# Optimization experiments

Hardware: AMD Instinct MI355X
Metric: run time of the kernel (lower is better)

## Reference

```python
import jax, jax.numpy as jnp
import numpy as np

PAD, UNK, START = 0, 1, 2
V, E, H = 32000, 256, 512   # vocab, emb dim, encoder hidden per direction
H2 = 2 * H                   # decoder hidden / encoder output dim
B, L, T = 32, 400, 64
OOV = 100


def _lstm(xe, Wi, Wh, b, reverse=False):
    """xe: [B,L,E] -> (hs [B,L,H], h_last [B,H])."""
    Bb = xe.shape[0]
    Hh = Wh.shape[0]
    def step(carry, xt):
        h, c = carry
        z = xt @ Wi + h @ Wh + b
        i, fg, g, o = jnp.split(z, 4, axis=-1)
        c = jax.nn.sigmoid(fg) * c + jax.nn.sigmoid(i) * jnp.tanh(g)
        h = jax.nn.sigmoid(o) * jnp.tanh(c)
        return (h, c), h
    init = (jnp.zeros((Bb, Hh), xe.dtype), jnp.zeros((Bb, Hh), xe.dtype))
    (hN, _), hs = jax.lax.scan(step, init, jnp.swapaxes(xe, 0, 1), reverse=reverse)
    return jnp.swapaxes(hs, 0, 1), hN


def _gru(x, h, Wi, Wh, b):
    D = h.shape[-1]
    zi = x @ Wi + b
    zh = h @ Wh
    r = jax.nn.sigmoid(zi[:, :D] + zh[:, :D])
    z = jax.nn.sigmoid(zi[:, D:2 * D] + zh[:, D:2 * D])
    n = jnp.tanh(zi[:, 2 * D:] + r * zh[:, 2 * D:])
    return (1.0 - z) * n + z * h


def _forward(embedding, enc_Wi_f, enc_Wh_f, enc_b_f, enc_Wi_b, enc_Wh_b, enc_b_b,
             dec_Wi, dec_Wh, dec_b, W_enc_att, W_dec_att, Wv, bv, Wp, bp,
             x, target_y, extend_vocab):
    Bb, Ll = x.shape
    Tt = target_y.shape[1]
    Vv = embedding.shape[0]
    Hh2 = dec_Wh.shape[0]
    xe = embedding[x]                                           # B,L,E
    hs_f, hN_f = _lstm(xe, enc_Wi_f, enc_Wh_f, enc_b_f)
    hs_b, hN_b = _lstm(xe, enc_Wi_b, enc_Wh_b, enc_b_b, reverse=True)
    enc_out = jnp.concatenate([hs_f, hs_b], axis=-1)            # B,L,2H
    dec_h0 = jnp.concatenate([hN_f, hN_b], axis=-1)             # B,2H
    bidx = jnp.arange(Bb)[:, None]

    def step(carry, inp):
        dec_in, dec_h, acc, prebuf = carry
        i, tgt = inp
        emb = embedding[dec_in]                                 # B,E
        dec_h = _gru(emb, dec_h, dec_Wi, dec_Wh, dec_b)         # B,2H
        # temporal encoder attention (normalize exp scores by running sum)
        e = jnp.einsum('bh,hk,blk->bl', dec_h, W_enc_att, enc_out)
        ee = jnp.exp(e)
        att_un = jnp.where(i == 0, ee, ee / (acc + 1e-10))
        acc = acc + ee
        enc_att = att_un / jnp.sum(att_un, axis=-1, keepdims=True)   # B,L
        enc_ctx = jnp.einsum('bl,blh->bh', enc_att, enc_out)
        # intra-decoder attention over previous decoder hiddens
        ed = jnp.einsum('bh,hk,btk->bt', dec_h, W_dec_att, prebuf)
        dmask = (jnp.arange(prebuf.shape[1]) < i)[None, :]
        dec_att = jax.nn.softmax(jnp.where(dmask, ed, -1e9), axis=-1)
        dec_ctx = jnp.einsum('bt,bth->bh', dec_att, prebuf)
        dec_ctx = jnp.where(i > 0, dec_ctx, 0.0)
        cat = jnp.concatenate([dec_h, enc_ctx, dec_ctx], axis=-1)    # B,6H
        p_gen = jax.nn.sigmoid(cat @ Wp + bp)                        # B,1
        ptr_dist = p_gen * enc_att                                   # B,L
        vocab_dist = (1.0 - p_gen) * jax.nn.softmax(cat @ Wv + bv, axis=-1)
        final = jnp.zeros((Bb, Vv + OOV), vocab_dist.dtype)
        final = final.at[:, :Vv].set(vocab_dist)
        final = final.at[bidx, extend_vocab].add(ptr_dist)           # copy mechanism
        dec_out = jnp.argmax(final, axis=-1)
        step_loss = -jnp.log(final[jnp.arange(Bb), tgt] + 1e-12)
        step_loss = step_loss * (tgt != PAD).astype(final.dtype)
        prebuf = jax.lax.dynamic_update_slice(prebuf, dec_h[:, None, :], (0, i, 0))
        nxt = jnp.where(dec_out >= Vv, UNK, dec_out).astype(dec_in.dtype)
        return (nxt, dec_h, acc, prebuf), (dec_out, step_loss)

    init = (jnp.full((Bb,), START, dtype=x.dtype), dec_h0,
            jnp.zeros((Bb, Ll), enc_out.dtype),
            jnp.zeros((Bb, Tt, Hh2), enc_out.dtype))
    _, (ys, losses) = jax.lax.scan(step, init, (jnp.arange(Tt), target_y.T))
    return jnp.swapaxes(ys, 0, 1), jnp.swapaxes(losses, 0, 1)


def setup_inputs() -> dict:
    key = jax.random.key(0)
    ks = jax.random.split(key, 16)
    s = 0.02
    nrm = lambda k, shape: jax.random.normal(k, shape, jnp.float32) * s
    return {
        'x': jax.random.randint(ks[0], (B, L), 0, V),
        'seq_len': L,
        'target_y': jax.random.randint(ks[1], (B, T), 0, V),
        'extend_vocab': jax.random.randint(ks[2], (B, L), 0, V + OOV),
        'max_ovv_len': OOV,
        'embedding': nrm(ks[3], (V, E)),
        'enc_Wi_f': nrm(ks[4], (E, 4 * H)),
        'enc_Wh_f': nrm(ks[5], (H, 4 * H)),
        'enc_b_f': jnp.zeros((4 * H,), jnp.float32),
        'enc_Wi_b': nrm(ks[6], (E, 4 * H)),
        'enc_Wh_b': nrm(ks[7], (H, 4 * H)),
        'enc_b_b': jnp.zeros((4 * H,), jnp.float32),
        'dec_Wi': nrm(ks[8], (E, 3 * H2)),
        'dec_Wh': nrm(ks[9], (H2, 3 * H2)),
        'dec_b': jnp.zeros((3 * H2,), jnp.float32),
        'W_enc_att': nrm(ks[10], (H2, H2)),
        'W_dec_att': nrm(ks[11], (H2, H2)),
        'Wv': nrm(ks[12], (3 * H2, V)),
        'bv': jnp.zeros((V,), jnp.float32),
        'Wp': nrm(ks[13], (3 * H2, 1)),
        'bp': jnp.zeros((1,), jnp.float32),
    }


def reference(x, seq_len, target_y, extend_vocab, max_ovv_len,
              embedding, enc_Wi_f, enc_Wh_f, enc_b_f, enc_Wi_b, enc_Wh_b, enc_b_b,
              dec_Wi, dec_Wh, dec_b, W_enc_att, W_dec_att, Wv, bv, Wp, bp):
    return _forward(embedding, enc_Wi_f, enc_Wh_f, enc_b_f, enc_Wi_b, enc_Wh_b, enc_b_b,
                    dec_Wi, dec_Wh, dec_b, W_enc_att, W_dec_att, Wv, bv, Wp, bp,
                    x, target_y, extend_vocab)
```

## Files before the change

kernel.cpp:

```cpp
#include <hip/hip_runtime.h>
#include <math.h>

#define Bb 32
#define Lmax 400
#define Tt 64
#define Ee 256
#define Hh 512
#define H2 1024
#define Vv 32000
#define OOV 100
#define VX (Vv+OOV)
#define PAD_ID 0
#define UNK_ID 1
#define START_ID 2

__device__ __forceinline__ float sigf(float x){ return 1.0f/(1.0f+expf(-x)); }
__device__ __forceinline__ float bf2f(unsigned int u){ u <<= 16; return __uint_as_float(u); }

__global__ __launch_bounds__(256) void pack_enc_k(
    const float* __restrict__ Wi_f, const float* __restrict__ Wh_f, const float* __restrict__ b_f,
    const float* __restrict__ Wi_b, const float* __restrict__ Wh_b, const float* __restrict__ b_b,
    float4* __restrict__ wip, float4* __restrict__ whp, float4* __restrict__ bp)
{
  int o = blockIdx.x*256 + threadIdx.x;
  if (o < 2*256*512) {
    int n = o & 511; int k = (o >> 9) & 255; int dir = o >> 17;
    const float* W = dir ? Wi_b : Wi_f;
    wip[o] = make_float4(W[k*2048+n], W[k*2048+512+n], W[k*2048+1024+n], W[k*2048+1536+n]);
  }
  if (o < 2*512*512) {
    int n = o & 511; int k = (o >> 9) & 511; int dir = o >> 18;
    const float* W = dir ? Wh_b : Wh_f;
    whp[o] = make_float4(W[k*2048+n], W[k*2048+512+n], W[k*2048+1024+n], W[k*2048+1536+n]);
  }
  if (o < 2*512) {
    int n = o & 511; int dir = o >> 9;
    const float* bs = dir ? b_b : b_f;
    bp[o] = make_float4(bs[n], bs[512+n], bs[1024+n], bs[1536+n]);
  }
}

#define FMA16(ACC, HV, W0, W1, W2, W3) \
  ACC.x = fmaf(HV.x, W0.x, ACC.x); ACC.y = fmaf(HV.x, W0.y, ACC.y); \
  ACC.z = fmaf(HV.x, W0.z, ACC.z); ACC.w = fmaf(HV.x, W0.w, ACC.w); \
  ACC.x = fmaf(HV.y, W1.x, ACC.x); ACC.y = fmaf(HV.y, W1.y, ACC.y); \
  ACC.z = fmaf(HV.y, W1.z, ACC.z); ACC.w = fmaf(HV.y, W1.w, ACC.w); \
  ACC.x = fmaf(HV.z, W2.x, ACC.x); ACC.y = fmaf(HV.z, W2.y, ACC.y); \
  ACC.z = fmaf(HV.z, W2.z, ACC.z); ACC.w = fmaf(HV.z, W2.w, ACC.w); \
  ACC.x = fmaf(HV.w, W3.x, ACC.x); ACC.y = fmaf(HV.w, W3.y, ACC.y); \
  ACC.z = fmaf(HV.w, W3.z, ACC.z); ACC.w = fmaf(HV.w, W3.w, ACC.w);

__global__ __launch_bounds__(512) void enc_step3_k(
    const float4* __restrict__ wip, const float4* __restrict__ whp, const float4* __restrict__ bp,
    const float* __restrict__ emb, const int* __restrict__ x,
    float* __restrict__ c_buf, float* __restrict__ enc_out, int t)
{
  __shared__ float4 wi_s[256*4];
  __shared__ float4 wh_s[512*4];
  __shared__ float4 hs2[128*33];
  __shared__ float4 xr_red[64*33];
  int bx = blockIdx.x;
  int dir = bx >> 7, ng = bx & 127;
  int tid = threadIdx.x;
  int ks = tid >> 5;
  int r  = tid & 31;
  int bq = r & 7, nl = r >> 3;
  int b0 = bq*4;
  int tt = dir ? (Lmax-1-t) : t;

  for (int i = tid; i < 1024; i += 512) {
    int k = i >> 2, l = i & 3;
    wi_s[i] = wip[(dir*256 + k)*512 + ng*4 + l];
  }
  for (int i = tid; i < 2048; i += 512) {
    int k = i >> 2, l = i & 3;
    wh_s[i] = whp[(dir*512 + k)*512 + ng*4 + l];
  }
  {
    int sb = tid >> 4, kb = tid & 15;
    int tok = x[sb*Lmax + tt];
    const float4* er = (const float4*)(emb + (size_t)tok*Ee);
    #pragma unroll
    for (int i = 0; i < 4; ++i) {
      int k4 = kb + 16*i;
      xr_red[k4*33 + sb] = er[k4];
    }
  }
  if (t > 0) {
    int pt = dir ? (tt+1) : (tt-1);
    int sb = tid >> 4, kb = tid & 15;
    const float4* hb = (const float4*)(enc_out + ((size_t)sb*Lmax + pt)*H2 + dir*Hh);
    #pragma unroll
    for (int i = 0; i < 8; ++i) {
      int k4 = kb + 16*i;
      hs2[k4*33 + sb] = hb[k4];
    }
  }
  __syncthreads();

  float4 acc0 = make_float4(0.f,0.f,0.f,0.f);
  float4 acc1 = acc0, acc2 = acc0, acc3 = acc0;
  if (t > 0) {
    int k4b = ks*8;
    #pragma unroll
    for (int kk = 0; kk < 8; ++kk) {
      int k4 = k4b + kk;
      float4 w0 = wh_s[(k4*4+0)*4 + nl];
      float4 w1 = wh_s[(k4*4+1)*4 + nl];
      float4 w2 = wh_s[(k4*4+2)*4 + nl];
      float4 w3 = wh_s[(k4*4+3)*4 + nl];
      float4 h0 = hs2[k4*33 + b0+0];
      float4 h1 = hs2[k4*33 + b0+1];
      float4 h2 = hs2[k4*33 + b0+2];
      float4 h3 = hs2[k4*33 + b0+3];
      FMA16(acc0, h0, w0, w1, w2, w3);
      FMA16(acc1, h1, w0, w1, w2, w3);
      FMA16(acc2, h2, w0, w1, w2, w3);
      FMA16(acc3, h3, w0, w1, w2, w3);
    }
  }
  {
    int k4b = ks*4;
    #pragma unroll
    for (int kk = 0; kk < 4; ++kk) {
      int k4 = k4b + kk;
      float4 w0 = wi_s[(k4*4+0)*4 + nl];
      float4 w1 = wi_s[(k4*4+1)*4 + nl];
      float4 w2 = wi_s[(k4*4+2)*4 + nl];
      float4 w3 = wi_s[(k4*4+3)*4 + nl];
      float4 h0 = xr_red[k4*33 + b0+0];
      float4 h1 = xr_red[k4*33 + b0+1];
      float4 h2 = xr_red[k4*33 + b0+2];
      float4 h3 = xr_red[k4*33 + b0+3];
      FMA16(acc0, h0, w0, w1, w2, w3);
      FMA16(acc1, h1, w0, w1, w2, w3);
      FMA16(acc2, h2, w0, w1, w2, w3);
      FMA16(acc3, h3, w0, w1, w2, w3);
    }
  }
  __syncthreads();
  {
    int base = ks*132 + 16*bq + nl;
    xr_red[base + 0]  = acc0;
    xr_red[base + 4]  = acc1;
    xr_red[base + 8]  = acc2;
    xr_red[base + 12] = acc3;
  }
  __syncthreads();
  if (tid < 128) {
    int bn = tid;
    float4 s = xr_red[bn];
    #pragma unroll
    for (int kr = 1; kr < 16; ++kr) {
      float4 v = xr_red[kr*132 + bn];
      s.x += v.x; s.y += v.y; s.z += v.z; s.w += v.w;
    }
    int b = bn >> 2, nl2 = bn & 3, n = ng*4 + nl2;
    float4 bb = bp[dir*512 + n];
    float zi = s.x + bb.x;
    float zf = s.y + bb.y;
    float zg = s.z + bb.z;
    float zo = s.w + bb.w;
    int ci = (dir*32 + b)*Hh + n;
    float cv = (t==0) ? 0.f : c_buf[ci];
    float cn = sigf(zf)*cv + sigf(zi)*tanhf(zg);
    float hn = sigf(zo)*tanhf(cn);
    c_buf[ci] = cn;
    enc_out[((size_t)b*Lmax + tt)*H2 + dir*Hh + n] = hn;
  }
}

__global__ __launch_bounds__(256) void init_dec_k(
    const float* __restrict__ enc_out, float* __restrict__ cat_buf,
    float* __restrict__ h0, int* __restrict__ dec_in)
{
  int idx = blockIdx.x*256 + threadIdx.x;
  if (idx < Bb*H2) {
    int b = idx >> 10, n = idx & 1023;
    float v = (n < Hh) ? enc_out[((size_t)b*Lmax + (Lmax-1))*H2 + n]
                       : enc_out[(size_t)b*Lmax*H2 + n];
    cat_buf[b*3*H2 + n] = v;
    h0[b*H2 + n] = v;
  }
  if (idx < Bb) dec_in[idx] = START_ID;
}

__global__ __launch_bounds__(256) void gru_mm_k(
    const float* __restrict__ emb, const int* __restrict__ dec_in,
    const float* __restrict__ cat_buf, const float* __restrict__ Wi,
    const float* __restrict__ Wh, const float* __restrict__ bias,
    float* __restrict__ zi_buf, float* __restrict__ zh_buf)
{
  int bx = blockIdx.x;
  int ng = bx % 48; int bg = (bx / 48) & 7; int kq = bx / 384;
  int nl = threadIdx.x & 63, bl = threadIdx.x >> 6;
  int n = ng*64 + nl, b = bg*4 + bl;
  const float* hr = cat_buf + b*3*H2;
  float zh = 0.f;
  int k0 = kq*512;
  #pragma unroll 4
  for (int k = k0; k < k0+512; ++k)
    zh = fmaf(hr[k], Wh[(size_t)k*3*H2 + n], zh);
  zh_buf[(size_t)(kq*Bb + b)*3*H2 + n] = zh;
  if (kq == 0) {
    const float* er = emb + (size_t)dec_in[b]*Ee;
    float zi = bias[n];
    #pragma unroll 4
    for (int k = 0; k < Ee; ++k)
      zi = fmaf(er[k], Wi[(size_t)k*3*H2 + n], zi);
    zi_buf[b*3*H2 + n] = zi;
  }
}

__global__ __launch_bounds__(256) void qq_f_k(
    const float* __restrict__ zi_buf, const float* __restrict__ zh_buf,
    const float* __restrict__ h0, float* __restrict__ prebuf,
    const float* __restrict__ Wea, const float* __restrict__ Wda,
    float* __restrict__ cat_buf, float* __restrict__ qp, float* __restrict__ qdp, int t)
{
  __shared__ float hsq[4*260];
  int bx = blockIdx.x;
  int ng = bx & 15, bg = (bx >> 4) & 7, kq = bx >> 7;
  int nl = threadIdx.x & 63, bl = threadIdx.x >> 6;
  int n = ng*64 + nl, b = bg*4 + bl;
  const float* zi  = zi_buf + b*3*H2;
  const float* zh0 = zh_buf + (size_t)b*3*H2;
  const float* zh1 = zh_buf + (size_t)(Bb + b)*3*H2;
  #pragma unroll
  for (int i = 0; i < 4; ++i) {
    int kk = nl + 64*i, k = kq*256 + kk;
    float zhr = zh0[k]      + zh1[k];
    float zhz = zh0[H2+k]   + zh1[H2+k];
    float zhg = zh0[2*H2+k] + zh1[2*H2+k];
    float rr = sigf(zi[k] + zhr);
    float zz = sigf(zi[H2+k] + zhz);
    float nn = tanhf(zi[2*H2+k] + rr*zhg);
    float hold = (t == 0) ? h0[b*H2 + k]
                          : prebuf[((size_t)b*Tt + (t-1))*H2 + k];
    float h = (1.0f - zz)*nn + zz*hold;
    hsq[bl*260 + kk] = h;
    if (ng == 0) {
      cat_buf[b*3*H2 + k] = h;
      prebuf[((size_t)b*Tt + t)*H2 + k] = h;
    }
  }
  __syncthreads();
  const float* hr = hsq + bl*260;
  const float* wa = Wea + (size_t)(kq*256)*H2 + n;
  const float* wd = Wda + (size_t)(kq*256)*H2 + n;
  float s1 = 0.f, s2 = 0.f;
  #pragma unroll 4
  for (int kk = 0; kk < 256; ++kk) {
    float hv = hr[kk];
    s1 = fmaf(hv, wa[(size_t)kk*H2], s1);
    s2 = fmaf(hv, wd[(size_t)kk*H2], s2);
  }
  qp [(size_t)(kq*Bb + b)*H2 + n] = s1;
  qdp[(size_t)(kq*Bb + b)*H2 + n] = s2;
}

__global__ __launch_bounds__(256) void qsum_k(
    const float* __restrict__ qp, const float* __restrict__ qdp,
    float* __restrict__ q, float* __restrict__ qd)
{
  int i = blockIdx.x*256 + threadIdx.x;
  const float4* p  = (const float4*)qp;
  const float4* pd = (const float4*)qdp;
  float4 a = p[i], b1 = p[8192+i], c = p[16384+i], d = p[24576+i];
  ((float4*)q)[i] = make_float4(a.x+b1.x+c.x+d.x, a.y+b1.y+c.y+d.y,
                                a.z+b1.z+c.z+d.z, a.w+b1.w+c.w+d.w);
  float4 e = pd[i], f = pd[8192+i], g = pd[16384+i], h = pd[24576+i];
  ((float4*)qd)[i] = make_float4(e.x+f.x+g.x+h.x, e.y+f.y+g.y+h.y,
                                 e.z+f.z+g.z+h.z, e.w+f.w+g.w+h.w);
}

__global__ __launch_bounds__(256) void att_sc_k(
    const float* __restrict__ q, const float* __restrict__ qd,
    const float* __restrict__ enc_out, const float* __restrict__ prebuf,
    float* __restrict__ esc, float* __restrict__ ed, int t)
{
  int w = blockIdx.x*4 + (threadIdx.x >> 6);
  int lane = threadIdx.x & 63;
  int b = w / 464;
  int row = w - b*464;
  if (b >= Bb) return;
  float s = 0.0f;
  if (row < Lmax) {
    const float4* qr = (const float4*)(q + b*H2);
    const float4* er = (const float4*)(enc_out + ((size_t)b*Lmax + row)*H2);
    #pragma unroll
    for (int j = 0; j < 4; ++j) {
      float4 a = qr[lane + 64*j], e = er[lane + 64*j];
      s += a.x*e.x + a.y*e.y + a.z*e.z + a.w*e.w;
    }
  } else {
    int tp = row - Lmax;
    if (tp >= t) { if (lane==0) ed[b*Tt+tp] = 0.0f; return; }
    const float4* qr = (const float4*)(qd + b*H2);
    const float4* pr = (const float4*)(prebuf + ((size_t)b*Tt + tp)*H2);
    #pragma unroll
    for (int j = 0; j < 4; ++j) {
      float4 a = qr[lane + 64*j], e = pr[lane + 64*j];
      s += a.x*e.x + a.y*e.y + a.z*e.z + a.w*e.w;
    }
  }
  for (int o = 32; o > 0; o >>= 1) s += __shfl_xor(s, o);
  if (lane == 0) { if (row < Lmax) esc[b*Lmax+row] = s; else ed[b*Tt + (row-Lmax)] = s; }
}

__global__ __launch_bounds__(256) void ctx_norm_k(
    const float* __restrict__ esc, const float* __restrict__ acc_r, float* __restrict__ acc_w,
    float* __restrict__ enc_att, const float* __restrict__ ed,
    const float* __restrict__ enc_out, const float* __restrict__ prebuf,
    float* __restrict__ cat_buf, int t)
{
  __shared__ float att_s[Lmax];
  __shared__ float datt_s[Tt];
  __shared__ float red[256];
  int b = blockIdx.x >> 4, kq = blockIdx.x & 15;
  int tid = threadIdx.x;
  float loc = 0.f;
  for (int l = tid; l < Lmax; l += 256) {
    float ee = expf(esc[b*Lmax + l]);
    float a  = (t == 0) ? 0.f : acc_r[b*Lmax + l];
    float un = (t == 0) ? ee : ee / (a + 1e-10f);
    att_s[l] = un;
    loc += un;
    if (kq == 0) acc_w[b*Lmax + l] = a + ee;
  }
  red[tid] = loc; __syncthreads();
  for (int s = 128; s > 0; s >>= 1) { if (tid < s) red[tid] += red[tid+s]; __syncthreads(); }
  float inv = 1.0f / red[0];
  for (int l = tid; l < Lmax; l += 256) {
    float v = att_s[l] * inv;
    att_s[l] = v;
    if (kq == 0) enc_att[b*Lmax + l] = v;
  }
  if (tid < 64 && t > 0) {
    float v = (tid < t) ? ed[b*Tt + tid] : -INFINITY;
    float m = v;
    for (int o = 32; o > 0; o >>= 1) m = fmaxf(m, __shfl_xor(m, o));
    float p = (tid < t) ? expf(v - m) : 0.f;
    float ss = p;
    for (int o = 32; o > 0; o >>= 1) ss += __shfl_xor(ss, o);
    datt_s[tid] = p / ss;
  }
  __syncthreads();
  int k = kq*64 + (tid & 63);
  int strip = tid >> 6;
  float ec = 0.f;
  const float* er = enc_out + (size_t)b*Lmax*H2 + k;
  #pragma unroll 4
  for (int l = strip; l < Lmax; l += 4)
    ec = fmaf(att_s[l], er[(size_t)l*H2], ec);
  float dc = 0.f;
  const float* pr = prebuf + (size_t)b*Tt*H2 + k;
  for (int tp = strip; tp < t; tp += 4)
    dc = fmaf(datt_s[tp], pr[(size_t)tp*H2], dc);
  __syncthreads();
  red[tid] = ec; __syncthreads();
  if (tid < 64)
    cat_buf[b*3*H2 + H2 + kq*64 + tid] = red[tid] + red[64+tid] + red[128+tid] + red[192+tid];
  __syncthreads();
  red[tid] = dc; __syncthreads();
  if (tid < 64)
    cat_buf[b*3*H2 + 2*H2 + kq*64 + tid] = red[tid] + red[64+tid] + red[128+tid] + red[192+tid];
}

__global__ __launch_bounds__(256) void pack_wv_k(const float* __restrict__ Wv, unsigned short* __restrict__ Wbf)
{
  size_t i = ((size_t)blockIdx.x*256 + threadIdx.x)*4;
  #pragma unroll
  for (int j = 0; j < 4; ++j) {
    unsigned int u = __float_as_uint(Wv[i+j]);
    u = (u + 0x7fffu + ((u >> 16) & 1u)) >> 16;
    Wbf[i+j] = (unsigned short)u;
  }
}

__global__ __launch_bounds__(256) void wv_mm_bf_k(
    const float* __restrict__ cat_buf, const unsigned short* __restrict__ Wbf,
    const float* __restrict__ bv, float* __restrict__ logits)
{
  __shared__ float As[32][33];
  __shared__ float Wsh[32][65];
  int tid = threadIdx.x;
  int n0 = blockIdx.x*64;
  int tx = tid & 15, ty = tid >> 4;
  float acc[2][4] = {};
  for (int k0 = 0; k0 < 3*H2; k0 += 32) {
    #pragma unroll
    for (int i = 0; i < 4; ++i) {
      int a = tid*4+i;
      As[a>>5][a&31] = cat_buf[(size_t)(a>>5)*3*H2 + k0 + (a&31)];
    }
    #pragma unroll
    for (int j = 0; j < 4; ++j) {
      int a = j*256 + tid;
      int row = a >> 5, c2 = (a & 31)*2;
      const unsigned int* wr = (const unsigned int*)(Wbf + (size_t)(k0+row)*Vv + n0);
      unsigned int u = wr[a & 31];
      Wsh[row][c2]   = bf2f(u & 0xffffu);
      Wsh[row][c2+1] = bf2f(u >> 16);
    }
    __syncthreads();
    #pragma unroll
    for (int kk = 0; kk < 32; ++kk) {
      float a0 = As[ty*2+0][kk], a1 = As[ty*2+1][kk];
      float w0 = Wsh[kk][tx*4+0], w1 = Wsh[kk][tx*4+1], w2 = Wsh[kk][tx*4+2], w3 = Wsh[kk][tx*4+3];
      acc[0][0]=fmaf(a0,w0,acc[0][0]); acc[0][1]=fmaf(a0,w1,acc[0][1]); acc[0][2]=fmaf(a0,w2,acc[0][2]); acc[0][3]=fmaf(a0,w3,acc[0][3]);
      acc[1][0]=fmaf(a1,w0,acc[1][0]); acc[1][1]=fmaf(a1,w1,acc[1][1]); acc[1][2]=fmaf(a1,w2,acc[1][2]); acc[1][3]=fmaf(a1,w3,acc[1][3]);
    }
    __syncthreads();
  }
  #pragma unroll
  for (int i = 0; i < 2; ++i)
    #pragma unroll
    for (int j = 0; j < 4; ++j) {
      int n = n0 + tx*4 + j;
      logits[(size_t)(ty*2+i)*Vv + n] = acc[i][j] + bv[n];
    }
}

__global__ __launch_bounds__(256) void wv_mm_k(
    const float* __restrict__ cat_buf, const float* __restrict__ Wv,
    const float* __restrict__ bv, float* __restrict__ logits)
{
  __shared__ float As[32][33];
  __shared__ float Wsh[32][128];
  int tid = threadIdx.x;
  int n0 = blockIdx.x*128;
  int tx = tid & 31, ty = tid >> 5;
  float acc[4][4] = {};
  for (int k0 = 0; k0 < 3*H2; k0 += 32) {
    #pragma unroll
    for (int i = 0; i < 4; ++i) {
      int a = tid*4+i;
      As[a>>5][a&31] = cat_buf[(size_t)(a>>5)*3*H2 + k0 + (a&31)];
    }
    #pragma unroll
    for (int j = 0; j < 16; ++j) {
      int a = j*256+tid;
      Wsh[a>>7][a&127] = Wv[(size_t)(k0+(a>>7))*Vv + n0 + (a&127)];
    }
    __syncthreads();
    #pragma unroll
    for (int kk = 0; kk < 32; ++kk) {
      float a0 = As[ty*4+0][kk], a1 = As[ty*4+1][kk], a2 = As[ty*4+2][kk], a3 = As[ty*4+3][kk];
      float w0 = Wsh[kk][tx*4+0], w1 = Wsh[kk][tx*4+1], w2 = Wsh[kk][tx*4+2], w3 = Wsh[kk][tx*4+3];
      acc[0][0]=fmaf(a0,w0,acc[0][0]); acc[0][1]=fmaf(a0,w1,acc[0][1]); acc[0][2]=fmaf(a0,w2,acc[0][2]); acc[0][3]=fmaf(a0,w3,acc[0][3]);
      acc[1][0]=fmaf(a1,w0,acc[1][0]); acc[1][1]=fmaf(a1,w1,acc[1][1]); acc[1][2]=fmaf(a1,w2,acc[1][2]); acc[1][3]=fmaf(a1,w3,acc[1][3]);
      acc[2][0]=fmaf(a2,w0,acc[2][0]); acc[2][1]=fmaf(a2,w1,acc[2][1]); acc[2][2]=fmaf(a2,w2,acc[2][2]); acc[2][3]=fmaf(a2,w3,acc[2][3]);
      acc[3][0]=fmaf(a3,w0,acc[3][0]); acc[3][1]=fmaf(a3,w1,acc[3][1]); acc[3][2]=fmaf(a3,w2,acc[3][2]); acc[3][3]=fmaf(a3,w3,acc[3][3]);
    }
    __syncthreads();
  }
  #pragma unroll
  for (int i = 0; i < 4; ++i)
    #pragma unroll
    for (int j = 0; j < 4; ++j) {
      int n = n0 + tx*4 + j;
      logits[(size_t)(ty*4+i)*Vv + n] = acc[i][j] + bv[n];
    }
}

__global__ __launch_bounds__(256) void final_k(
    const float* __restrict__ logits, const float* __restrict__ cat_buf,
    const float* __restrict__ Wp, const float* __restrict__ bps,
    const int* __restrict__ ev, const float* __restrict__ enc_att,
    const int* __restrict__ tgt_y, float* __restrict__ out,
    int* __restrict__ dec_in, int t)
{
  __shared__ float rf[256];
  __shared__ int   ri[256];
  __shared__ float tm[256];
  __shared__ int   ev_s[Lmax];
  __shared__ float pv_s[Lmax];
  __shared__ float m_sh, sc_sh, pg_sh;
  int b = blockIdx.x, tid = threadIdx.x;
  const float*  lr  = logits + (size_t)b*Vv;
  const float4* lr4 = (const float4*)lr;
  {
    const float* catr = cat_buf + b*3*H2;
    float pgl = 0.f;
    for (int i = tid; i < 3*H2; i += 256) pgl += catr[i]*Wp[i];
    rf[tid] = pgl; __syncthreads();
    for (int s = 128; s > 0; s >>= 1) { if (tid < s) rf[tid] += rf[tid+s]; __syncthreads(); }
    if (tid == 0) pg_sh = sigf(rf[0] + bps[0]);
    __syncthreads();
  }
  float m = -1e30f;
  for (int i = tid; i < Vv/4; i += 256) {
    float4 v = lr4[i];
    m = fmaxf(m, fmaxf(fmaxf(v.x,v.y), fmaxf(v.z,v.w)));
  }
  rf[tid] = m; __syncthreads();
  for (int s = 128; s > 0; s >>= 1) { if (tid < s) rf[tid] = fmaxf(rf[tid], rf[tid+s]); __syncthreads(); }
  m = rf[0]; __syncthreads();
  float ssum = 0.f;
  for (int i = tid; i < Vv/4; i += 256) {
    float4 v = lr4[i];
    ssum += expf(v.x-m) + expf(v.y-m) + expf(v.z-m) + expf(v.w-m);
  }
  rf[tid] = ssum; __syncthreads();
  for (int s = 128; s > 0; s >>= 1) { if (tid < s) rf[tid] += rf[tid+s]; __syncthreads(); }
  if (tid == 0) {
    sc_sh = (1.0f - pg_sh) / rf[0]; m_sh = m;
  }
  for (int l = tid; l < Lmax; l += 256) ev_s[l] = ev[b*Lmax + l];
  __syncthreads();
  float scale = sc_sh, pg = pg_sh; m = m_sh;
  for (int l = tid; l < Lmax; l += 256) pv_s[l] = pg * enc_att[b*Lmax + l];
  __syncthreads();
  float best = -1e30f; int bi = 0x7fffffff;
  for (int i = tid; i < Vv/4; i += 256) {
    float4 v = lr4[i];
    float p0 = expf(v.x-m)*scale, p1 = expf(v.y-m)*scale, p2 = expf(v.z-m)*scale, p3 = expf(v.w-m)*scale;
    int n = 4*i;
    if (p0 > best) { best = p0; bi = n; }
    if (p1 > best || (p1 == best && n+1 < bi)) { best = p1; bi = n+1; }
    if (p2 > best || (p2 == best && n+2 < bi)) { best = p2; bi = n+2; }
    if (p3 > best || (p3 == best && n+3 < bi)) { best = p3; bi = n+3; }
  }
  int tgt = tgt_y[b*Tt + t];
  float ptm = 0.f;
  for (int l = tid; l < Lmax; l += 256) {
    int e = ev_s[l];
    float tot = 0.f;
    for (int l2 = 0; l2 < Lmax; ++l2) if (ev_s[l2] == e) tot += pv_s[l2];
    float vvv = tot + ((e < Vv) ? expf(lr[e]-m)*scale : 0.f);
    if (vvv > best || (vvv == best && e < bi)) { best = vvv; bi = e; }
    ptm += (e == tgt) ? pv_s[l] : 0.f;
  }
  rf[tid] = best; ri[tid] = bi; tm[tid] = ptm; __syncthreads();
  for (int s = 128; s > 0; s >>= 1) {
    if (tid < s) {
      float v2 = rf[tid+s]; int i2 = ri[tid+s];
      if (v2 > rf[tid] || (v2 == rf[tid] && i2 < ri[tid])) { rf[tid] = v2; ri[tid] = i2; }
      tm[tid] += tm[tid+s];
    }
    __syncthreads();
  }
  if (tid == 0) {
    int am = ri[0];
    float fr_tgt = expf(lr[tgt]-m)*scale + tm[0];
    float loss = (tgt != PAD_ID) ? -logf(fr_tgt + 1e-12f) : 0.0f;
    out[b*Tt + t] = (float)am;
    out[Bb*Tt + b*Tt + t] = loss;
    dec_in[b] = (am >= Vv) ? UNK_ID : am;
  }
}

extern "C" void kernel_launch(void* const* d_in, const int* in_sizes, int n_in,
                              void* d_out, int out_size, void* d_ws, size_t ws_size,
                              hipStream_t stream)
{
  const int*   x    = (const int*)  d_in[0];
  const int*   tgt  = (const int*)  d_in[2];
  const int*   ev   = (const int*)  d_in[3];
  const float* emb  = (const float*)d_in[5];
  const float* Wi_f = (const float*)d_in[6];
  const float* Wh_f = (const float*)d_in[7];
  const float* b_f  = (const float*)d_in[8];
  const float* Wi_b = (const float*)d_in[9];
  const float* Wh_b = (const float*)d_in[10];
  const float* b_b  = (const float*)d_in[11];
  const float* dWi  = (const float*)d_in[12];
  const float* dWh  = (const float*)d_in[13];
  const float* db   = (const float*)d_in[14];
  const float* Wea  = (const float*)d_in[15];
  const float* Wda  = (const float*)d_in[16];
  const float* Wv   = (const float*)d_in[17];
  const float* bv   = (const float*)d_in[18];
  const float* Wp   = (const float*)d_in[19];
  const float* bp   = (const float*)d_in[20];
  float* out = (float*)d_out;

  float* ws = (float*)d_ws;
  size_t off = 0;
  float* enc_out = ws + off; off += (size_t)Bb*Lmax*H2;
  float* c_buf   = ws + off; off += 2*Bb*Hh;
  float4* wip    = (float4*)(ws + off); off += 2*256*512*4;
  float4* whp    = (float4*)(ws + off); off += 2*512*512*4;
  float4* biasp  = (float4*)(ws + off); off += 2*512*4;
  float* cat_buf = ws + off; off += Bb*3*H2;
  float* prebuf  = ws + off; off += (size_t)Bb*Tt*H2;
  float* accumA  = ws + off; off += Bb*Lmax;
  float* accumB  = ws + off; off += Bb*Lmax;
  float* zi_buf  = ws + off; off += Bb*3*H2;
  float* zh_buf  = ws + off; off += (size_t)2*Bb*3*H2;
  float* qp      = ws + off; off += (size_t)4*Bb*H2;
  float* qdp     = ws + off; off += (size_t)4*Bb*H2;
  float* q       = ws + off; off += Bb*H2;
  float* qd      = ws + off; off += Bb*H2;
  float* h0      = ws + off; off += Bb*H2;
  float* esc     = ws + off; off += Bb*Lmax;
  float* enc_att = ws + off; off += Bb*Lmax;
  float* ed      = ws + off; off += Bb*Tt;
  float* logits  = ws + off; off += (size_t)Bb*Vv;
  int*   dec_in  = (int*)(ws + off); off += 32;
  unsigned short* Wbf = (unsigned short*)(ws + off);
  size_t need_bf16 = off*4 + (size_t)3*H2*Vv*2;
  int use_bf16 = (ws_size >= need_bf16 + (64u<<10)) ? 1 : 0;

  pack_enc_k<<<2048,256,0,stream>>>(Wi_f,Wh_f,b_f,Wi_b,Wh_b,b_b,wip,whp,biasp);
  if (use_bf16) pack_wv_k<<<96000,256,0,stream>>>(Wv, Wbf);

  for (int t = 0; t < Lmax; ++t)
    enc_step3_k<<<256,512,0,stream>>>(wip,whp,biasp,emb,x,c_buf,enc_out,t);

  init_dec_k<<<128,256,0,stream>>>(enc_out,cat_buf,h0,dec_in);

  for (int t = 0; t < Tt; ++t) {
    float* ar = (t & 1) ? accumB : accumA;
    float* aw = (t & 1) ? accumA : accumB;
    gru_mm_k  <<<768,256,0,stream>>>(emb,dec_in,cat_buf,dWi,dWh,db,zi_buf,zh_buf);
    qq_f_k    <<<512,256,0,stream>>>(zi_buf,zh_buf,h0,prebuf,Wea,Wda,cat_buf,qp,qdp,t);
    qsum_k    <<<32,256,0,stream>>>(qp,qdp,q,qd);
    att_sc_k  <<<3712,256,0,stream>>>(q,qd,enc_out,prebuf,esc,ed,t);
    ctx_norm_k<<<512,256,0,stream>>>(esc,ar,aw,enc_att,ed,enc_out,prebuf,cat_buf,t);
    if (use_bf16) wv_mm_bf_k<<<500,256,0,stream>>>(cat_buf,Wbf,bv,logits);
    else          wv_mm_k   <<<250,256,0,stream>>>(cat_buf,Wv,bv,logits);
    final_k   <<<32,256,0,stream>>>(logits,cat_buf,Wp,bp,ev,enc_att,tgt,out,dec_in,t);
  }
}
```

Before: 34.72 ms.

## Run encoder LSTM as one persistent kernel with a global atomic barrier

```diff
diff --git a/kernel.cpp b/kernel.cpp
--- a/kernel.cpp
+++ b/kernel.cpp
@@ -20,9 +20,11 @@
 __global__ __launch_bounds__(256) void pack_enc_k(
     const float* __restrict__ Wi_f, const float* __restrict__ Wh_f, const float* __restrict__ b_f,
     const float* __restrict__ Wi_b, const float* __restrict__ Wh_b, const float* __restrict__ b_b,
-    float4* __restrict__ wip, float4* __restrict__ whp, float4* __restrict__ bp)
+    float4* __restrict__ wip, float4* __restrict__ whp, float4* __restrict__ bp,
+    unsigned* __restrict__ ctr)
 {
   int o = blockIdx.x*256 + threadIdx.x;
+  if (o == 0) ctr[0] = 0u;
   if (o < 2*256*512) {
     int n = o & 511; int k = (o >> 9) & 255; int dir = o >> 17;
     const float* W = dir ? Wi_b : Wi_f;
@@ -49,6 +51,139 @@
   ACC.z = fmaf(HV.z, W2.z, ACC.z); ACC.w = fmaf(HV.z, W2.w, ACC.w); \
   ACC.x = fmaf(HV.w, W3.x, ACC.x); ACC.y = fmaf(HV.w, W3.y, ACC.y); \
   ACC.z = fmaf(HV.w, W3.z, ACC.z); ACC.w = fmaf(HV.w, W3.w, ACC.w);
+
+__global__ __launch_bounds__(512, 1) void enc_persist_k(
+    const float4* __restrict__ wip, const float4* __restrict__ whp, const float4* __restrict__ bp,
+    const float* __restrict__ emb, const int* __restrict__ x,
+    float* __restrict__ enc_out, unsigned* __restrict__ ctr)
+{
+  __shared__ float4 wi_s[256*4];
+  __shared__ float4 wh_s[512*4];
+  __shared__ float4 hs2[128*33];
+  __shared__ float4 xr_red[64*33];
+  int bx = blockIdx.x;
+  int dir = bx >> 7, ng = bx & 127;
+  int tid = threadIdx.x;
+  int ks = tid >> 5;
+  int r  = tid & 31;
+  int bq = r & 7, nl = r >> 3;
+  int b0 = bq*4;
+  int sb = tid >> 4, kb = tid & 15;
+
+  for (int i = tid; i < 1024; i += 512) {
+    int k = i >> 2, l = i & 3;
+    wi_s[i] = wip[(dir*256 + k)*512 + ng*4 + l];
+  }
+  for (int i = tid; i < 2048; i += 512) {
+    int k = i >> 2, l = i & 3;
+    wh_s[i] = whp[(dir*512 + k)*512 + ng*4 + l];
+  }
+  float c_reg = 0.f;
+  float4 bb = make_float4(0.f,0.f,0.f,0.f);
+  if (tid < 128) bb = bp[dir*512 + ng*4 + (tid & 3)];
+
+  for (int t = 0; t < Lmax; ++t) {
+    int tt = dir ? (Lmax-1-t) : t;
+    {
+      int tok = x[sb*Lmax + tt];
+      const float4* er = (const float4*)(emb + (size_t)tok*Ee);
+      #pragma unroll
+      for (int i = 0; i < 4; ++i) {
+        int k4 = kb + 16*i;
+        xr_red[k4*33 + sb] = er[k4];
+      }
+    }
+    if (t > 0) {
+      int pt = dir ? (tt+1) : (tt-1);
+      const float4* hb = (const float4*)(enc_out + ((size_t)sb*Lmax + pt)*H2 + dir*Hh);
+      #pragma unroll
+      for (int i = 0; i < 8; ++i) {
+        int k4 = kb + 16*i;
+        hs2[k4*33 + sb] = hb[k4];
+      }
+    }
+    __syncthreads();
+
+    float4 acc0 = make_float4(0.f,0.f,0.f,0.f);
+    float4 acc1 = acc0, acc2 = acc0, acc3 = acc0;
+    if (t > 0) {
+      int k4b = ks*8;
+      #pragma unroll
+      for (int kk = 0; kk < 8; ++kk) {
+        int k4 = k4b + kk;
+        float4 w0 = wh_s[(k4*4+0)*4 + nl];
+        float4 w1 = wh_s[(k4*4+1)*4 + nl];
+        float4 w2 = wh_s[(k4*4+2)*4 + nl];
+        float4 w3 = wh_s[(k4*4+3)*4 + nl];
+        float4 h0 = hs2[k4*33 + b0+0];
+        float4 h1 = hs2[k4*33 + b0+1];
+        float4 h2 = hs2[k4*33 + b0+2];
+        float4 h3 = hs2[k4*33 + b0+3];
+        FMA16(acc0, h0, w0, w1, w2, w3);
+        FMA16(acc1, h1, w0, w1, w2, w3);
+        FMA16(acc2, h2, w0, w1, w2, w3);
+        FMA16(acc3, h3, w0, w1, w2, w3);
+      }
+    }
+    {
+      int k4b = ks*4;
+      #pragma unroll
+      for (int kk = 0; kk < 4; ++kk) {
+        int k4 = k4b + kk;
+        float4 w0 = wi_s[(k4*4+0)*4 + nl];
+        float4 w1 = wi_s[(k4*4+1)*4 + nl];
+        float4 w2 = wi_s[(k4*4+2)*4 + nl];
+        float4 w3 = wi_s[(k4*4+3)*4 + nl];
+        float4 h0 = xr_red[k4*33 + b0+0];
+        float4 h1 = xr_red[k4*33 + b0+1];
+        float4 h2 = xr_red[k4*33 + b0+2];
+        float4 h3 = xr_red[k4*33 + b0+3];
+        FMA16(acc0, h0, w0, w1, w2, w3);
+        FMA16(acc1, h1, w0, w1, w2, w3);
+        FMA16(acc2, h2, w0, w1, w2, w3);
+        FMA16(acc3, h3, w0, w1, w2, w3);
+      }
+    }
+    __syncthreads();
+    {
+      int base = ks*132 + 16*bq + nl;
+      xr_red[base + 0]  = acc0;
+      xr_red[base + 4]  = acc1;
+      xr_red[base + 8]  = acc2;
+      xr_red[base + 12] = acc3;
+    }
+    __syncthreads();
+    if (tid < 128) {
+      int bn = tid;
+      float4 s = xr_red[bn];
+      #pragma unroll
+      for (int kr = 1; kr < 16; ++kr) {
+        float4 v = xr_red[kr*132 + bn];
+        s.x += v.x; s.y += v.y; s.z += v.z; s.w += v.w;
+      }
+      int b = bn >> 2, nl2 = bn & 3, n = ng*4 + nl2;
+      float zi = s.x + bb.x;
+      float zf = s.y + bb.y;
+      float zg = s.z + bb.z;
+      float zo = s.w + bb.w;
+      float cn = sigf(zf)*c_reg + sigf(zi)*tanhf(zg);
+      float hn = sigf(zo)*tanhf(cn);
+      c_reg = cn;
+      enc_out[((size_t)b*Lmax + tt)*H2 + dir*Hh + n] = hn;
+    }
+    __syncthreads();
+    if (t < Lmax-1) {
+      if (tid == 0) {
+        __hip_atomic_fetch_add(ctr, 1u, __ATOMIC_RELEASE, __HIP_MEMORY_SCOPE_AGENT);
+        unsigned tgt = 256u * (unsigned)(t+1);
+        while (__hip_atomic_load(ctr, __ATOMIC_RELAXED, __HIP_MEMORY_SCOPE_AGENT) < tgt)
+          __builtin_amdgcn_s_sleep(16);
+        (void)__hip_atomic_load(ctr, __ATOMIC_ACQUIRE, __HIP_MEMORY_SCOPE_AGENT);
+      }
+      __syncthreads();
+    }
+  }
+}
 
 __global__ __launch_bounds__(512) void enc_step3_k(
     const float4* __restrict__ wip, const float4* __restrict__ whp, const float4* __restrict__ bp,
@@ -67,7 +202,6 @@
   int bq = r & 7, nl = r >> 3;
   int b0 = bq*4;
   int tt = dir ? (Lmax-1-t) : t;
-
   for (int i = tid; i < 1024; i += 512) {
     int k = i >> 2, l = i & 3;
     wi_s[i] = wip[(dir*256 + k)*512 + ng*4 + l];
@@ -97,7 +231,6 @@
     }
   }
   __syncthreads();
-
   float4 acc0 = make_float4(0.f,0.f,0.f,0.f);
   float4 acc1 = acc0, acc2 = acc0, acc3 = acc0;
   if (t > 0) {
@@ -427,11 +560,11 @@
     const float* __restrict__ bv, float* __restrict__ logits)
 {
   __shared__ float As[32][33];
-  __shared__ float Wsh[32][128];
+  __shared__ float Wsh[32][65];
   int tid = threadIdx.x;
-  int n0 = blockIdx.x*128;
-  int tx = tid & 31, ty = tid >> 5;
-  float acc[4][4] = {};
+  int n0 = blockIdx.x*64;
+  int tx = tid & 15, ty = tid >> 4;
+  float acc[2][4] = {};
   for (int k0 = 0; k0 < 3*H2; k0 += 32) {
     #pragma unroll
     for (int i = 0; i < 4; ++i) {
@@ -439,28 +572,27 @@
       As[a>>5][a&31] = cat_buf[(size_t)(a>>5)*3*H2 + k0 + (a&31)];
     }
     #pragma unroll
-    for (int j = 0; j < 16; ++j) {
-      int a = j*256+tid;
-      Wsh[a>>7][a&127] = Wv[(size_t)(k0+(a>>7))*Vv + n0 + (a&127)];
+    for (int j = 0; j < 8; ++j) {
+      int a = j*256 + tid;
+      int row = a >> 6, col = a & 63;
+      Wsh[row][col] = Wv[(size_t)(k0+row)*Vv + n0 + col];
     }
     __syncthreads();
     #pragma unroll
     for (int kk = 0; kk < 32; ++kk) {
-      float a0 = As[ty*4+0][kk], a1 = As[ty*4+1][kk], a2 = As[ty*4+2][kk], a3 = As[ty*4+3][kk];
+      float a0 = As[ty*2+0][kk], a1 = As[ty*2+1][kk];
       float w0 = Wsh[kk][tx*4+0], w1 = Wsh[kk][tx*4+1], w2 = Wsh[kk][tx*4+2], w3 = Wsh[kk][tx*4+3];
       acc[0][0]=fmaf(a0,w0,acc[0][0]); acc[0][1]=fmaf(a0,w1,acc[0][1]); acc[0][2]=fmaf(a0,w2,acc[0][2]); acc[0][3]=fmaf(a0,w3,acc[0][3]);
       acc[1][0]=fmaf(a1,w0,acc[1][0]); acc[1][1]=fmaf(a1,w1,acc[1][1]); acc[1][2]=fmaf(a1,w2,acc[1][2]); acc[1][3]=fmaf(a1,w3,acc[1][3]);
-      acc[2][0]=fmaf(a2,w0,acc[2][0]); acc[2][1]=fmaf(a2,w1,acc[2][1]); acc[2][2]=fmaf(a2,w2,acc[2][2]); acc[2][3]=fmaf(a2,w3,acc[2][3]);
-      acc[3][0]=fmaf(a3,w0,acc[3][0]); acc[3][1]=fmaf(a3,w1,acc[3][1]); acc[3][2]=fmaf(a3,w2,acc[3][2]); acc[3][3]=fmaf(a3,w3,acc[3][3]);
     }
     __syncthreads();
   }
   #pragma unroll
-  for (int i = 0; i < 4; ++i)
+  for (int i = 0; i < 2; ++i)
     #pragma unroll
     for (int j = 0; j < 4; ++j) {
       int n = n0 + tx*4 + j;
-      logits[(size_t)(ty*4+i)*Vv + n] = acc[i][j] + bv[n];
+      logits[(size_t)(ty*2+i)*Vv + n] = acc[i][j] + bv[n];
     }
 }
 
@@ -576,13 +708,43 @@
   const float* bp   = (const float*)d_in[20];
   float* out = (float*)d_out;
 
+  static int g_persist = -1;
+  if (g_persist < 0) {
+    int dev = 0; (void)hipGetDevice(&dev);
+    int mp = 0;
+    if (hipDeviceGetAttribute(&mp, hipDeviceAttributeMultiprocessorCount, dev) != hipSuccess) mp = 0;
+    g_persist = (mp >= 256) ? 1 : 0;
+  }
+
   float* ws = (float*)d_ws;
-  size_t off = 0;
-  float* enc_out = ws + off; off += (size_t)Bb*Lmax*H2;
-  float* c_buf   = ws + off; off += 2*Bb*Hh;
-  float4* wip    = (float4*)(ws + off); off += 2*256*512*4;
-  float4* whp    = (float4*)(ws + off); off += 2*512*512*4;
-  float4* biasp  = (float4*)(ws + off); off += 2*512*4;
+  size_t head_enc = (size_t)Bb*Lmax*H2;
+  size_t head_c   = 2*Bb*Hh;
+  size_t head = head_enc + head_c;
+  size_t wgt_floats = (size_t)2*256*512*4 + (size_t)2*512*512*4 + (size_t)2*512*4;
+  size_t wbf_floats = (size_t)3*H2*Vv/2;
+  const size_t REST =
+      (size_t)Bb*3*H2
+    + (size_t)Bb*Tt*H2
+    + 2*(size_t)Bb*Lmax
+    + (size_t)Bb*3*H2
+    + (size_t)2*Bb*3*H2
+    + (size_t)8*Bb*H2
+    + (size_t)3*Bb*H2
+    + 2*(size_t)Bb*Lmax
+    + (size_t)Bb*Tt
+    + (size_t)Bb*Vv
+    + 64;
+  int use_bf16 = (ws_size >= (head + wbf_floats + REST)*4 + (64u<<10)) ? 1 : 0;
+  size_t mid = use_bf16 ? wbf_floats : wgt_floats;
+
+  float* enc_out = ws;
+  float* c_buf   = ws + head_enc;
+  float4* wip    = (float4*)(ws + head);
+  float4* whp    = (float4*)(ws + head + (size_t)2*256*512*4);
+  float4* biasp  = (float4*)(ws + head + (size_t)2*256*512*4 + (size_t)2*512*512*4);
+  unsigned short* Wbf = (unsigned short*)(ws + head);
+
+  size_t off = head + mid;
   float* cat_buf = ws + off; off += Bb*3*H2;
   float* prebuf  = ws + off; off += (size_t)Bb*Tt*H2;
   float* accumA  = ws + off; off += Bb*Lmax;
@@ -599,15 +761,18 @@
   float* ed      = ws + off; off += Bb*Tt;
   float* logits  = ws + off; off += (size_t)Bb*Vv;
   int*   dec_in  = (int*)(ws + off); off += 32;
-  unsigned short* Wbf = (unsigned short*)(ws + off);
-  size_t need_bf16 = off*4 + (size_t)3*H2*Vv*2;
-  int use_bf16 = (ws_size >= need_bf16 + (64u<<10)) ? 1 : 0;
-
-  pack_enc_k<<<2048,256,0,stream>>>(Wi_f,Wh_f,b_f,Wi_b,Wh_b,b_b,wip,whp,biasp);
+  unsigned* ctr  = (unsigned*)(ws + off); off += 32;
+
+  pack_enc_k<<<2048,256,0,stream>>>(Wi_f,Wh_f,b_f,Wi_b,Wh_b,b_b,wip,whp,biasp,ctr);
+
+  if (g_persist) {
+    enc_persist_k<<<256,512,0,stream>>>(wip,whp,biasp,emb,x,enc_out,ctr);
+  } else {
+    for (int t = 0; t < Lmax; ++t)
+      enc_step3_k<<<256,512,0,stream>>>(wip,whp,biasp,emb,x,c_buf,enc_out,t);
+  }
+
   if (use_bf16) pack_wv_k<<<96000,256,0,stream>>>(Wv, Wbf);
-
-  for (int t = 0; t < Lmax; ++t)
-    enc_step3_k<<<256,512,0,stream>>>(wip,whp,biasp,emb,x,c_buf,enc_out,t);
 
   init_dec_k<<<128,256,0,stream>>>(enc_out,cat_buf,h0,dec_in);
 
@@ -620,7 +785,7 @@
     att_sc_k  <<<3712,256,0,stream>>>(q,qd,enc_out,prebuf,esc,ed,t);
     ctx_norm_k<<<512,256,0,stream>>>(esc,ar,aw,enc_att,ed,enc_out,prebuf,cat_buf,t);
     if (use_bf16) wv_mm_bf_k<<<500,256,0,stream>>>(cat_buf,Wbf,bv,logits);
-    else          wv_mm_k   <<<250,256,0,stream>>>(cat_buf,Wv,bv,logits);
+    else          wv_mm_k   <<<500,256,0,stream>>>(cat_buf,Wv,bv,logits);
     final_k   <<<32,256,0,stream>>>(logits,cat_buf,Wp,bp,ev,enc_att,tgt,out,dec_in,t);
   }
 }
```

After: 38.13 ms. 9.8% more time.
